# Kernel tuning notes

Hardware: AMD Instinct MI355X
Metric: run time of the kernel (lower is better)

Reference implementation:

```python
import jax, jax.numpy as jnp
import numpy as np

LATENT, HIDDEN, OUT, NBLOCKS, NITER, BATCH = 128, 256, 128, 4, 10, 65536

def setup_inputs() -> dict:
    key = jax.random.key(0)
    ks = jax.random.split(key, 7)
    s_in = 1.0 / np.sqrt(LATENT)
    s_h = 1.0 / np.sqrt(HIDDEN)
    return {
        "x": jax.random.normal(ks[0], (BATCH, LATENT), jnp.float32),
        "W_init": jax.random.uniform(ks[1], (LATENT, HIDDEN), jnp.float32, -s_in, s_in),
        "b_init": jnp.zeros((HIDDEN,), jnp.float32),
        "Wg1": jax.random.uniform(ks[2], (NBLOCKS, HIDDEN, HIDDEN), jnp.float32, -s_h, s_h),
        "bg1": jax.random.uniform(ks[3], (NBLOCKS, HIDDEN), jnp.float32, -s_h, s_h),
        "Wg2": jax.random.uniform(ks[4], (NBLOCKS, HIDDEN, HIDDEN), jnp.float32, -s_h, s_h),
        "bg2": jax.random.uniform(ks[5], (NBLOCKS, HIDDEN), jnp.float32, -s_h, s_h),
        "W_final": jax.random.uniform(ks[6], (HIDDEN, OUT), jnp.float32, -s_h, s_h),
        "b_final": jnp.zeros((OUT,), jnp.float32),
    }

def _block(y, W1, b1, W2, b2):
    # fixed-point iteration: x <- y - g(x), g = Linear-ReLU-Linear
    def step(x, _):
        g = jax.nn.relu(x @ W1 + b1) @ W2 + b2
        return y - g, None
    x, _ = jax.lax.scan(step, y, None, length=NITER)
    return x

def reference(x, W_init, b_init, Wg1, bg1, Wg2, bg2, W_final, b_final):
    h = x @ W_init + b_init  # [B, HIDDEN]
    def blk(h, params):
        W1, b1, W2, b2 = params
        return _block(h, W1, b1, W2, b2), None
    h, _ = jax.lax.scan(blk, h, (Wg1, bg1, Wg2, bg2))
    return h @ W_final + b_final
```

## Files before the change

### kernel.cpp

```cpp
#include <hip/hip_runtime.h>
#include <hip/hip_bf16.h>


#define B_TOTAL 65536
#define LATENT  128
#define HIDDEN  256
#define OUTD    128
#define NBLOCKS 4
#define NITER   10
#define MTILE   64
#define LDSP    264

typedef unsigned short u16;
typedef unsigned int   u32;
typedef u16    u16x4  __attribute__((ext_vector_type(4)));
typedef u16    u16x8  __attribute__((ext_vector_type(8)));
typedef __bf16 bf16x8 __attribute__((ext_vector_type(8)));
typedef float  f32x16 __attribute__((ext_vector_type(16)));

__device__ inline u16 f2b(float f){ __bf16 h=(__bf16)f; return __builtin_bit_cast(u16,h); }
__device__ inline float up_lo(u32 u){ return __builtin_bit_cast(float, u<<16); }
__device__ inline float up_hi(u32 u){ return __builtin_bit_cast(float, u & 0xffff0000u); }
__device__ inline u32 pk2(float lo, float hi){ return (u32)f2b(lo) | ((u32)f2b(hi)<<16); }

#define AGC \
 "a0","a1","a2","a3","a4","a5","a6","a7","a8","a9","a10","a11","a12","a13","a14","a15", \
 "a16","a17","a18","a19","a20","a21","a22","a23","a24","a25","a26","a27","a28","a29","a30","a31", \
 "a32","a33","a34","a35","a36","a37","a38","a39","a40","a41","a42","a43","a44","a45","a46","a47", \
 "a48","a49","a50","a51","a52","a53","a54","a55","a56","a57","a58","a59","a60","a61","a62","a63", \
 "a64","a65","a66","a67","a68","a69","a70","a71","a72","a73","a74","a75","a76","a77","a78","a79", \
 "a80","a81","a82","a83","a84","a85","a86","a87","a88","a89","a90","a91","a92","a93","a94","a95", \
 "a96","a97","a98","a99","a100","a101","a102","a103","a104","a105","a106","a107","a108","a109","a110","a111", \
 "a112","a113","a114","a115","a116","a117","a118","a119","a120","a121","a122","a123","a124","a125","a126","a127"

#define LOADW(P, KS, NEG, A0,A1,A2,A3) { \
  const float* _w = (P) + (size_t)((KS)*16 + hi*8)*HIDDEN + colw; \
  float _v0=_w[0], _v1=_w[HIDDEN], _v2=_w[2*HIDDEN], _v3=_w[3*HIDDEN]; \
  float _v4=_w[4*HIDDEN], _v5=_w[5*HIDDEN], _v6=_w[6*HIDDEN], _v7=_w[7*HIDDEN]; \
  if (NEG){_v0=-_v0;_v1=-_v1;_v2=-_v2;_v3=-_v3;_v4=-_v4;_v5=-_v5;_v6=-_v6;_v7=-_v7;} \
  u32 _d0=pk2(_v0,_v1), _d1=pk2(_v2,_v3), _d2=pk2(_v4,_v5), _d3=pk2(_v6,_v7); \
  asm volatile("v_accvgpr_write_b32 a" #A0 ", %0\n\t" \
               "v_accvgpr_write_b32 a" #A1 ", %1\n\t" \
               "v_accvgpr_write_b32 a" #A2 ", %2\n\t" \
               "v_accvgpr_write_b32 a" #A3 ", %3" \
               :: "v"(_d0),"v"(_d1),"v"(_d2),"v"(_d3) : AGC); }

#define STEP(SRC, KS, A0, A3) { \
  bf16x8 _b0 = *(const bf16x8*)((SRC) + rdA0 + (KS)*16); \
  bf16x8 _b1 = *(const bf16x8*)((SRC) + rdA1 + (KS)*16); \
  asm volatile("v_mfma_f32_32x32x16_bf16 %0, a[" #A0 ":" #A3 "], %1, %0" \
               : "+v"(acc0) : "v"(_b0) : AGC); \
  asm volatile("v_mfma_f32_32x32x16_bf16 %0, a[" #A0 ":" #A3 "], %1, %0" \
               : "+v"(acc1) : "v"(_b1) : AGC); }

#define ACCFENCE asm volatile("s_nop 7\n\ts_nop 7\n\ts_nop 7" : "+v"(acc0), "+v"(acc1))

#define MFMA_I(a,b,c) __builtin_amdgcn_mfma_f32_32x32x16_bf16(a,b,c,0,0,0)

__device__ inline bf16x8 load_wfrag_f(const float* __restrict__ W, int ldw, int krow0,
                                      int col){
  bf16x8 r;
#pragma unroll
  for (int j=0;j<8;j++) r[j] = (__bf16)W[(size_t)(krow0+j)*ldw + col];
  return r;
}

__device__ inline void store_tile(u16* __restrict__ dst, int row_elem, int nb, int hi,
                                  const f32x16 a, bool relu){
#pragma unroll
  for (int q=0;q<4;q++){
    u16x4 p;
#pragma unroll
    for (int i=0;i<4;i++){
      float v = a[4*q+i];
      if (relu) v = v > 0.f ? v : 0.f;
      p[i] = f2b(v);
    }
    *(u16x4*)(dst + row_elem + nb + 8*q + 4*hi) = p;
  }
}

__global__
__attribute__((amdgpu_flat_work_group_size(512,512)))
void irn_kernel(const float* __restrict__ x,
                const float* __restrict__ Winit, const float* __restrict__ binit,
                const float* __restrict__ Wg1,   const float* __restrict__ bg1,
                const float* __restrict__ Wg2,   const float* __restrict__ bg2,
                const float* __restrict__ Wfin,  const float* __restrict__ bfin,
                float* __restrict__ out)
{
  __shared__ u16 Xb[MTILE*LDSP];
  __shared__ u16 Hb[MTILE*LDSP];

  const int tid = threadIdx.x;
  const int wv  = tid >> 6;
  const int ln  = tid & 63;
  const int lo  = ln & 31;
  const int hi  = ln >> 5;
  const int row0 = blockIdx.x * MTILE;
  const int nb   = wv * 32;
  const int colw = nb + lo;

  {
    const int r  = tid >> 3;
    const int c0 = (tid & 7) * 16;
    const float4* src = (const float4*)(x + (size_t)(row0 + r)*LATENT + c0);
    u16x8 p0, p1;
#pragma unroll
    for (int i=0;i<2;i++){
      float4 a = src[i*2], b = src[i*2+1];
      u16x8& p = i ? p1 : p0;
      p[0]=f2b(a.x); p[1]=f2b(a.y); p[2]=f2b(a.z); p[3]=f2b(a.w);
      p[4]=f2b(b.x); p[5]=f2b(b.y); p[6]=f2b(b.z); p[7]=f2b(b.w);
    }
    u16* dst = Xb + r*LDSP + c0;
    *(u16x8*)(dst)   = p0;
    *(u16x8*)(dst+8) = p1;
  }

  const int rdA0 = lo*LDSP + hi*8;
  const int rdA1 = (32+lo)*LDSP + hi*8;

  u32 yp0[8], yp1[8];
  u32 b1p[8];

  __syncthreads();

  {
    bf16x8 wf[8];
#pragma unroll
    for (int ks=0; ks<8; ks++)
      wf[ks] = load_wfrag_f(Winit, HIDDEN, ks*16 + hi*8, colw);
    f32x16 acc0, acc1;
#pragma unroll
    for (int r=0;r<16;r++){
      float bv = binit[nb + (r&3) + 8*(r>>2) + 4*hi];
      acc0[r]=bv; acc1[r]=bv;
    }
#pragma unroll
    for (int ks=0; ks<8; ks++){
      bf16x8 b0 = *(const bf16x8*)(Xb + rdA0 + ks*16);
      bf16x8 b1 = *(const bf16x8*)(Xb + rdA1 + ks*16);
      acc0=MFMA_I(wf[ks], b0, acc0);
      acc1=MFMA_I(wf[ks], b1, acc1);
    }
    __syncthreads();
    store_tile(Xb, (0 +lo)*LDSP, nb, hi, acc0, false);
    store_tile(Xb, (32+lo)*LDSP, nb, hi, acc1, false);
#pragma unroll
    for (int i=0;i<8;i++){
      yp0[i] = pk2(acc0[2*i], acc0[2*i+1]);
      yp1[i] = pk2(acc1[2*i], acc1[2*i+1]);
    }
    __syncthreads();
  }

#pragma unroll 1
  for (int b=0; b<NBLOCKS; b++){
    const float* W1p = Wg1 + (size_t)b*HIDDEN*HIDDEN;
    const float* W2p = Wg2 + (size_t)b*HIDDEN*HIDDEN;

    LOADW(W1p, 0,0,  0,1,2,3)    LOADW(W1p, 1,0,  4,5,6,7)
    LOADW(W1p, 2,0,  8,9,10,11)  LOADW(W1p, 3,0,  12,13,14,15)
    LOADW(W1p, 4,0,  16,17,18,19) LOADW(W1p, 5,0,  20,21,22,23)
    LOADW(W1p, 6,0,  24,25,26,27) LOADW(W1p, 7,0,  28,29,30,31)
    LOADW(W1p, 8,0,  32,33,34,35) LOADW(W1p, 9,0,  36,37,38,39)
    LOADW(W1p,10,0,  40,41,42,43) LOADW(W1p,11,0,  44,45,46,47)
    LOADW(W1p,12,0,  48,49,50,51) LOADW(W1p,13,0,  52,53,54,55)
    LOADW(W1p,14,0,  56,57,58,59) LOADW(W1p,15,0,  60,61,62,63)
    LOADW(W2p, 0,1,  64,65,66,67)   LOADW(W2p, 1,1,  68,69,70,71)
    LOADW(W2p, 2,1,  72,73,74,75)   LOADW(W2p, 3,1,  76,77,78,79)
    LOADW(W2p, 4,1,  80,81,82,83)   LOADW(W2p, 5,1,  84,85,86,87)
    LOADW(W2p, 6,1,  88,89,90,91)   LOADW(W2p, 7,1,  92,93,94,95)
    LOADW(W2p, 8,1,  96,97,98,99)   LOADW(W2p, 9,1,  100,101,102,103)
    LOADW(W2p,10,1,  104,105,106,107) LOADW(W2p,11,1,  108,109,110,111)
    LOADW(W2p,12,1,  112,113,114,115) LOADW(W2p,13,1,  116,117,118,119)
    LOADW(W2p,14,1,  120,121,122,123) LOADW(W2p,15,1,  124,125,126,127)
    asm volatile("s_nop 3" :::);

    {
      const float* b1g = bg1 + b*HIDDEN;
      const float* b2g = bg2 + b*HIDDEN;
#pragma unroll
      for (int i=0;i<8;i++){
        const int c = nb + (2*i&3) + 8*(2*i>>2) + 4*hi;
        b1p[i] = pk2(b1g[c], b1g[c+1]);
        yp0[i] = pk2(up_lo(yp0[i]) - b2g[c], up_hi(yp0[i]) - b2g[c+1]);
        yp1[i] = pk2(up_lo(yp1[i]) - b2g[c], up_hi(yp1[i]) - b2g[c+1]);
      }
    }

#pragma unroll 1
    for (int it=0; it<NITER; it++){
      {
        f32x16 acc0, acc1;
#pragma unroll
        for (int i=0;i<8;i++){
          acc0[2*i]=up_lo(b1p[i]); acc0[2*i+1]=up_hi(b1p[i]);
          acc1[2*i]=acc0[2*i];     acc1[2*i+1]=acc0[2*i+1];
        }
        STEP(Xb, 0, 0,3)   STEP(Xb, 1, 4,7)   STEP(Xb, 2, 8,11)  STEP(Xb, 3, 12,15)
        STEP(Xb, 4, 16,19) STEP(Xb, 5, 20,23) STEP(Xb, 6, 24,27) STEP(Xb, 7, 28,31)
        STEP(Xb, 8, 32,35) STEP(Xb, 9, 36,39) STEP(Xb,10, 40,43) STEP(Xb,11, 44,47)
        STEP(Xb,12, 48,51) STEP(Xb,13, 52,55) STEP(Xb,14, 56,59) STEP(Xb,15, 60,63)
        ACCFENCE;
        store_tile(Hb, (0 +lo)*LDSP, nb, hi, acc0, true);
        store_tile(Hb, (32+lo)*LDSP, nb, hi, acc1, true);
      }
      __syncthreads();
      {
        f32x16 acc0, acc1;
#pragma unroll
        for (int i=0;i<8;i++){
          acc0[2*i]=up_lo(yp0[i]); acc0[2*i+1]=up_hi(yp0[i]);
          acc1[2*i]=up_lo(yp1[i]); acc1[2*i+1]=up_hi(yp1[i]);
        }
        STEP(Hb, 0, 64,67)   STEP(Hb, 1, 68,71)   STEP(Hb, 2, 72,75)   STEP(Hb, 3, 76,79)
        STEP(Hb, 4, 80,83)   STEP(Hb, 5, 84,87)   STEP(Hb, 6, 88,91)   STEP(Hb, 7, 92,95)
        STEP(Hb, 8, 96,99)   STEP(Hb, 9, 100,103) STEP(Hb,10, 104,107) STEP(Hb,11, 108,111)
        STEP(Hb,12, 112,115) STEP(Hb,13, 116,119) STEP(Hb,14, 120,123) STEP(Hb,15, 124,127)
        ACCFENCE;
        store_tile(Xb, (0 +lo)*LDSP, nb, hi, acc0, false);
        store_tile(Xb, (32+lo)*LDSP, nb, hi, acc1, false);
        if (it == NITER-1){
#pragma unroll
          for (int i=0;i<8;i++){
            yp0[i] = pk2(acc0[2*i], acc0[2*i+1]);
            yp1[i] = pk2(acc1[2*i], acc1[2*i+1]);
          }
        }
      }
      __syncthreads();
    }
  }

  {
    const int mf = (wv & 3) * 32;
    const int nf = (wv >> 2);
    const int rdF = (nf*32 + lo)*LDSP + hi*8;
    bf16x8 wf[16];
#pragma unroll
    for (int ks=0; ks<16; ks++)
      wf[ks] = load_wfrag_f(Wfin, OUTD, ks*16 + hi*8, mf + lo);
    f32x16 acc;
#pragma unroll
    for (int r=0;r<16;r++) acc[r] = bfin[mf + (r&3) + 8*(r>>2) + 4*hi];
#pragma unroll
    for (int ks=0; ks<16; ks++){
      bf16x8 bfr = *(const bf16x8*)(Xb + rdF + ks*16);
      acc = MFMA_I(wf[ks], bfr, acc);
    }
    float* orow = out + (size_t)(row0 + nf*32 + lo)*OUTD;
#pragma unroll
    for (int q=0;q<4;q++){
      float4 v = make_float4(acc[4*q], acc[4*q+1], acc[4*q+2], acc[4*q+3]);
      *(float4*)(orow + mf + 8*q + 4*hi) = v;
    }
  }
}

extern "C" void kernel_launch(void* const* d_in, const int* in_sizes, int n_in,
                              void* d_out, int out_size, void* d_ws, size_t ws_size,
                              hipStream_t stream) {
  (void)in_sizes; (void)n_in; (void)d_ws; (void)ws_size; (void)out_size;
  const float* x     = (const float*)d_in[0];
  const float* Winit = (const float*)d_in[1];
  const float* binit = (const float*)d_in[2];
  const float* Wg1   = (const float*)d_in[3];
  const float* bg1   = (const float*)d_in[4];
  const float* Wg2   = (const float*)d_in[5];
  const float* bg2   = (const float*)d_in[6];
  const float* Wfin  = (const float*)d_in[7];
  const float* bfin  = (const float*)d_in[8];
  float* out = (float*)d_out;
  irn_kernel<<<dim3(B_TOTAL/MTILE), dim3(512), 0, stream>>>(
      x, Winit, binit, Wg1, bg1, Wg2, bg2, Wfin, bfin, out);
}
```

Measured before the change: 768.4 us.

## Halve workgroup to 4 waves, each computing a 64x64 output tile

The workgroup shrinks from 8 waves to 4, and each wave now handles 64 output columns (two 32-column weight fragments) instead of 32. This doubles MFMA work per wave for every LDS B-fragment read, cutting LDS read traffic per FLOP. The hand-written AGPR inline-asm weight pinning is replaced with compiler-managed register arrays: 64 bf16x8 weight fragments per wave, plus waves_per_eu(1,1) so the compiler can use the full register file. The risks are register spills, lower occupancy, and the loss of explicit AGPR placement.

```diff
diff --git a/kernel.cpp b/kernel.cpp
--- a/kernel.cpp
+++ b/kernel.cpp
@@ -23,39 +23,17 @@
 __device__ inline float up_hi(u32 u){ return __builtin_bit_cast(float, u & 0xffff0000u); }
 __device__ inline u32 pk2(float lo, float hi){ return (u32)f2b(lo) | ((u32)f2b(hi)<<16); }
 
-#define AGC \
- "a0","a1","a2","a3","a4","a5","a6","a7","a8","a9","a10","a11","a12","a13","a14","a15", \
- "a16","a17","a18","a19","a20","a21","a22","a23","a24","a25","a26","a27","a28","a29","a30","a31", \
- "a32","a33","a34","a35","a36","a37","a38","a39","a40","a41","a42","a43","a44","a45","a46","a47", \
- "a48","a49","a50","a51","a52","a53","a54","a55","a56","a57","a58","a59","a60","a61","a62","a63", \
- "a64","a65","a66","a67","a68","a69","a70","a71","a72","a73","a74","a75","a76","a77","a78","a79", \
- "a80","a81","a82","a83","a84","a85","a86","a87","a88","a89","a90","a91","a92","a93","a94","a95", \
- "a96","a97","a98","a99","a100","a101","a102","a103","a104","a105","a106","a107","a108","a109","a110","a111", \
- "a112","a113","a114","a115","a116","a117","a118","a119","a120","a121","a122","a123","a124","a125","a126","a127"
-
-#define LOADW(P, KS, NEG, A0,A1,A2,A3) { \
-  const float* _w = (P) + (size_t)((KS)*16 + hi*8)*HIDDEN + colw; \
-  float _v0=_w[0], _v1=_w[HIDDEN], _v2=_w[2*HIDDEN], _v3=_w[3*HIDDEN]; \
-  float _v4=_w[4*HIDDEN], _v5=_w[5*HIDDEN], _v6=_w[6*HIDDEN], _v7=_w[7*HIDDEN]; \
-  if (NEG){_v0=-_v0;_v1=-_v1;_v2=-_v2;_v3=-_v3;_v4=-_v4;_v5=-_v5;_v6=-_v6;_v7=-_v7;} \
-  u32 _d0=pk2(_v0,_v1), _d1=pk2(_v2,_v3), _d2=pk2(_v4,_v5), _d3=pk2(_v6,_v7); \
-  asm volatile("v_accvgpr_write_b32 a" #A0 ", %0\n\t" \
-               "v_accvgpr_write_b32 a" #A1 ", %1\n\t" \
-               "v_accvgpr_write_b32 a" #A2 ", %2\n\t" \
-               "v_accvgpr_write_b32 a" #A3 ", %3" \
-               :: "v"(_d0),"v"(_d1),"v"(_d2),"v"(_d3) : AGC); }
-
-#define STEP(SRC, KS, A0, A3) { \
-  bf16x8 _b0 = *(const bf16x8*)((SRC) + rdA0 + (KS)*16); \
-  bf16x8 _b1 = *(const bf16x8*)((SRC) + rdA1 + (KS)*16); \
-  asm volatile("v_mfma_f32_32x32x16_bf16 %0, a[" #A0 ":" #A3 "], %1, %0" \
-               : "+v"(acc0) : "v"(_b0) : AGC); \
-  asm volatile("v_mfma_f32_32x32x16_bf16 %0, a[" #A0 ":" #A3 "], %1, %0" \
-               : "+v"(acc1) : "v"(_b1) : AGC); }
-
-#define ACCFENCE asm volatile("s_nop 7\n\ts_nop 7\n\ts_nop 7" : "+v"(acc0), "+v"(acc1))
-
 #define MFMA_I(a,b,c) __builtin_amdgcn_mfma_f32_32x32x16_bf16(a,b,c,0,0,0)
+
+__device__ inline bf16x8 wfrag(const float* __restrict__ W, int krow0, int col, bool neg){
+  bf16x8 r;
+#pragma unroll
+  for (int j=0;j<8;j++){
+    float v = W[(size_t)(krow0+j)*HIDDEN + col];
+    r[j] = (__bf16)(neg ? -v : v);
+  }
+  return r;
+}
 
 __device__ inline bf16x8 load_wfrag_f(const float* __restrict__ W, int ldw, int krow0,
                                       int col){
@@ -65,7 +43,7 @@
   return r;
 }
 
-__device__ inline void store_tile(u16* __restrict__ dst, int row_elem, int nb, int hi,
+__device__ inline void store_tile(u16* __restrict__ dst, int row_elem, int colbase, int hi,
                                   const f32x16 a, bool relu){
 #pragma unroll
   for (int q=0;q<4;q++){
@@ -76,12 +54,12 @@
       if (relu) v = v > 0.f ? v : 0.f;
       p[i] = f2b(v);
     }
-    *(u16x4*)(dst + row_elem + nb + 8*q + 4*hi) = p;
+    *(u16x4*)(dst + row_elem + colbase + 8*q + 4*hi) = p;
   }
 }
 
 __global__
-__attribute__((amdgpu_flat_work_group_size(512,512)))
+__attribute__((amdgpu_flat_work_group_size(256,256), amdgpu_waves_per_eu(1,1)))
 void irn_kernel(const float* __restrict__ x,
                 const float* __restrict__ Winit, const float* __restrict__ binit,
                 const float* __restrict__ Wg1,   const float* __restrict__ bg1,
@@ -98,59 +76,69 @@
   const int lo  = ln & 31;
   const int hi  = ln >> 5;
   const int row0 = blockIdx.x * MTILE;
-  const int nb   = wv * 32;
-  const int colw = nb + lo;
+  const int nb   = wv * 64;
+  const int colw0 = nb + lo;
+  const int colw1 = nb + 32 + lo;
 
   {
-    const int r  = tid >> 3;
-    const int c0 = (tid & 7) * 16;
+    const int r  = tid >> 2;
+    const int c0 = (tid & 3) * 32;
     const float4* src = (const float4*)(x + (size_t)(row0 + r)*LATENT + c0);
-    u16x8 p0, p1;
-#pragma unroll
-    for (int i=0;i<2;i++){
+    u16* dst = Xb + r*LDSP + c0;
+#pragma unroll
+    for (int i=0;i<4;i++){
       float4 a = src[i*2], b = src[i*2+1];
-      u16x8& p = i ? p1 : p0;
+      u16x8 p;
       p[0]=f2b(a.x); p[1]=f2b(a.y); p[2]=f2b(a.z); p[3]=f2b(a.w);
       p[4]=f2b(b.x); p[5]=f2b(b.y); p[6]=f2b(b.z); p[7]=f2b(b.w);
-    }
-    u16* dst = Xb + r*LDSP + c0;
-    *(u16x8*)(dst)   = p0;
-    *(u16x8*)(dst+8) = p1;
+      *(u16x8*)(dst + i*8) = p;
+    }
   }
 
   const int rdA0 = lo*LDSP + hi*8;
   const int rdA1 = (32+lo)*LDSP + hi*8;
 
-  u32 yp0[8], yp1[8];
-  u32 b1p[8];
+  u32 yp00[8], yp10[8], yp01[8], yp11[8];
+  u32 b1p0[8], b1p1[8];
 
   __syncthreads();
 
   {
-    bf16x8 wf[8];
-#pragma unroll
-    for (int ks=0; ks<8; ks++)
-      wf[ks] = load_wfrag_f(Winit, HIDDEN, ks*16 + hi*8, colw);
-    f32x16 acc0, acc1;
+    bf16x8 wf0[8], wf1[8];
+#pragma unroll
+    for (int ks=0; ks<8; ks++){
+      wf0[ks] = load_wfrag_f(Winit, HIDDEN, ks*16 + hi*8, colw0);
+      wf1[ks] = load_wfrag_f(Winit, HIDDEN, ks*16 + hi*8, colw1);
+    }
+    f32x16 acc00, acc10, acc01, acc11;
 #pragma unroll
     for (int r=0;r<16;r++){
-      float bv = binit[nb + (r&3) + 8*(r>>2) + 4*hi];
-      acc0[r]=bv; acc1[r]=bv;
+      const int cm = (r&3) + 8*(r>>2) + 4*hi;
+      float bv0 = binit[nb + cm];
+      float bv1 = binit[nb + 32 + cm];
+      acc00[r]=bv0; acc10[r]=bv0;
+      acc01[r]=bv1; acc11[r]=bv1;
     }
 #pragma unroll
     for (int ks=0; ks<8; ks++){
       bf16x8 b0 = *(const bf16x8*)(Xb + rdA0 + ks*16);
       bf16x8 b1 = *(const bf16x8*)(Xb + rdA1 + ks*16);
-      acc0=MFMA_I(wf[ks], b0, acc0);
-      acc1=MFMA_I(wf[ks], b1, acc1);
+      acc00=MFMA_I(wf0[ks], b0, acc00);
+      acc10=MFMA_I(wf0[ks], b1, acc10);
+      acc01=MFMA_I(wf1[ks], b0, acc01);
+      acc11=MFMA_I(wf1[ks], b1, acc11);
     }
     __syncthreads();
-    store_tile(Xb, (0 +lo)*LDSP, nb, hi, acc0, false);
-    store_tile(Xb, (32+lo)*LDSP, nb, hi, acc1, false);
+    store_tile(Xb, (0 +lo)*LDSP, nb,    hi, acc00, false);
+    store_tile(Xb, (32+lo)*LDSP, nb,    hi, acc10, false);
+    store_tile(Xb, (0 +lo)*LDSP, nb+32, hi, acc01, false);
+    store_tile(Xb, (32+lo)*LDSP, nb+32, hi, acc11, false);
 #pragma unroll
     for (int i=0;i<8;i++){
-      yp0[i] = pk2(acc0[2*i], acc0[2*i+1]);
-      yp1[i] = pk2(acc1[2*i], acc1[2*i+1]);
+      yp00[i] = pk2(acc00[2*i], acc00[2*i+1]);
+      yp10[i] = pk2(acc10[2*i], acc10[2*i+1]);
+      yp01[i] = pk2(acc01[2*i], acc01[2*i+1]);
+      yp11[i] = pk2(acc11[2*i], acc11[2*i+1]);
     }
     __syncthreads();
   }
@@ -160,73 +148,87 @@
     const float* W1p = Wg1 + (size_t)b*HIDDEN*HIDDEN;
     const float* W2p = Wg2 + (size_t)b*HIDDEN*HIDDEN;
 
-    LOADW(W1p, 0,0,  0,1,2,3)    LOADW(W1p, 1,0,  4,5,6,7)
-    LOADW(W1p, 2,0,  8,9,10,11)  LOADW(W1p, 3,0,  12,13,14,15)
-    LOADW(W1p, 4,0,  16,17,18,19) LOADW(W1p, 5,0,  20,21,22,23)
-    LOADW(W1p, 6,0,  24,25,26,27) LOADW(W1p, 7,0,  28,29,30,31)
-    LOADW(W1p, 8,0,  32,33,34,35) LOADW(W1p, 9,0,  36,37,38,39)
-    LOADW(W1p,10,0,  40,41,42,43) LOADW(W1p,11,0,  44,45,46,47)
-    LOADW(W1p,12,0,  48,49,50,51) LOADW(W1p,13,0,  52,53,54,55)
-    LOADW(W1p,14,0,  56,57,58,59) LOADW(W1p,15,0,  60,61,62,63)
-    LOADW(W2p, 0,1,  64,65,66,67)   LOADW(W2p, 1,1,  68,69,70,71)
-    LOADW(W2p, 2,1,  72,73,74,75)   LOADW(W2p, 3,1,  76,77,78,79)
-    LOADW(W2p, 4,1,  80,81,82,83)   LOADW(W2p, 5,1,  84,85,86,87)
-    LOADW(W2p, 6,1,  88,89,90,91)   LOADW(W2p, 7,1,  92,93,94,95)
-    LOADW(W2p, 8,1,  96,97,98,99)   LOADW(W2p, 9,1,  100,101,102,103)
-    LOADW(W2p,10,1,  104,105,106,107) LOADW(W2p,11,1,  108,109,110,111)
-    LOADW(W2p,12,1,  112,113,114,115) LOADW(W2p,13,1,  116,117,118,119)
-    LOADW(W2p,14,1,  120,121,122,123) LOADW(W2p,15,1,  124,125,126,127)
-    asm volatile("s_nop 3" :::);
+    bf16x8 wA[16], wB[16], wC[16], wD[16];
+#pragma unroll
+    for (int ks=0; ks<16; ks++){
+      const int kr = ks*16 + hi*8;
+      wA[ks] = wfrag(W1p, kr, colw0, false);
+      wB[ks] = wfrag(W1p, kr, colw1, false);
+      wC[ks] = wfrag(W2p, kr, colw0, true);
+      wD[ks] = wfrag(W2p, kr, colw1, true);
+    }
 
     {
       const float* b1g = bg1 + b*HIDDEN;
       const float* b2g = bg2 + b*HIDDEN;
 #pragma unroll
       for (int i=0;i<8;i++){
-        const int c = nb + (2*i&3) + 8*(2*i>>2) + 4*hi;
-        b1p[i] = pk2(b1g[c], b1g[c+1]);
-        yp0[i] = pk2(up_lo(yp0[i]) - b2g[c], up_hi(yp0[i]) - b2g[c+1]);
-        yp1[i] = pk2(up_lo(yp1[i]) - b2g[c], up_hi(yp1[i]) - b2g[c+1]);
+        const int cm = (2*i&3) + 8*(2*i>>2) + 4*hi;
+        const int c0 = nb + cm, c1 = nb + 32 + cm;
+        b1p0[i] = pk2(b1g[c0], b1g[c0+1]);
+        b1p1[i] = pk2(b1g[c1], b1g[c1+1]);
+        yp00[i] = pk2(up_lo(yp00[i]) - b2g[c0], up_hi(yp00[i]) - b2g[c0+1]);
+        yp10[i] = pk2(up_lo(yp10[i]) - b2g[c0], up_hi(yp10[i]) - b2g[c0+1]);
+        yp01[i] = pk2(up_lo(yp01[i]) - b2g[c1], up_hi(yp01[i]) - b2g[c1+1]);
+        yp11[i] = pk2(up_lo(yp11[i]) - b2g[c1], up_hi(yp11[i]) - b2g[c1+1]);
       }
     }
 
 #pragma unroll 1
     for (int it=0; it<NITER; it++){
       {
-        f32x16 acc0, acc1;
+        f32x16 acc00, acc10, acc01, acc11;
 #pragma unroll
         for (int i=0;i<8;i++){
-          acc0[2*i]=up_lo(b1p[i]); acc0[2*i+1]=up_hi(b1p[i]);
-          acc1[2*i]=acc0[2*i];     acc1[2*i+1]=acc0[2*i+1];
-        }
-        STEP(Xb, 0, 0,3)   STEP(Xb, 1, 4,7)   STEP(Xb, 2, 8,11)  STEP(Xb, 3, 12,15)
-        STEP(Xb, 4, 16,19) STEP(Xb, 5, 20,23) STEP(Xb, 6, 24,27) STEP(Xb, 7, 28,31)
-        STEP(Xb, 8, 32,35) STEP(Xb, 9, 36,39) STEP(Xb,10, 40,43) STEP(Xb,11, 44,47)
-        STEP(Xb,12, 48,51) STEP(Xb,13, 52,55) STEP(Xb,14, 56,59) STEP(Xb,15, 60,63)
-        ACCFENCE;
-        store_tile(Hb, (0 +lo)*LDSP, nb, hi, acc0, true);
-        store_tile(Hb, (32+lo)*LDSP, nb, hi, acc1, true);
+          acc00[2*i]=up_lo(b1p0[i]); acc00[2*i+1]=up_hi(b1p0[i]);
+          acc10[2*i]=acc00[2*i];     acc10[2*i+1]=acc00[2*i+1];
+          acc01[2*i]=up_lo(b1p1[i]); acc01[2*i+1]=up_hi(b1p1[i]);
+          acc11[2*i]=acc01[2*i];     acc11[2*i+1]=acc01[2*i+1];
+        }
+#pragma unroll
+        for (int ks=0; ks<16; ks++){
+          bf16x8 b0 = *(const bf16x8*)(Xb + rdA0 + ks*16);
+          bf16x8 b1 = *(const bf16x8*)(Xb + rdA1 + ks*16);
+          acc00 = MFMA_I(wA[ks], b0, acc00);
+          acc10 = MFMA_I(wA[ks], b1, acc10);
+          acc01 = MFMA_I(wB[ks], b0, acc01);
+          acc11 = MFMA_I(wB[ks], b1, acc11);
+        }
+        store_tile(Hb, (0 +lo)*LDSP, nb,    hi, acc00, true);
+        store_tile(Hb, (32+lo)*LDSP, nb,    hi, acc10, true);
+        store_tile(Hb, (0 +lo)*LDSP, nb+32, hi, acc01, true);
+        store_tile(Hb, (32+lo)*LDSP, nb+32, hi, acc11, true);
       }
       __syncthreads();
       {
-        f32x16 acc0, acc1;
+        f32x16 acc00, acc10, acc01, acc11;
 #pragma unroll
         for (int i=0;i<8;i++){
-          acc0[2*i]=up_lo(yp0[i]); acc0[2*i+1]=up_hi(yp0[i]);
-          acc1[2*i]=up_lo(yp1[i]); acc1[2*i+1]=up_hi(yp1[i]);
-        }
-        STEP(Hb, 0, 64,67)   STEP(Hb, 1, 68,71)   STEP(Hb, 2, 72,75)   STEP(Hb, 3, 76,79)
-        STEP(Hb, 4, 80,83)   STEP(Hb, 5, 84,87)   STEP(Hb, 6, 88,91)   STEP(Hb, 7, 92,95)
-        STEP(Hb, 8, 96,99)   STEP(Hb, 9, 100,103) STEP(Hb,10, 104,107) STEP(Hb,11, 108,111)
-        STEP(Hb,12, 112,115) STEP(Hb,13, 116,119) STEP(Hb,14, 120,123) STEP(Hb,15, 124,127)
-        ACCFENCE;
-        store_tile(Xb, (0 +lo)*LDSP, nb, hi, acc0, false);
-        store_tile(Xb, (32+lo)*LDSP, nb, hi, acc1, false);
+          acc00[2*i]=up_lo(yp00[i]); acc00[2*i+1]=up_hi(yp00[i]);
+          acc10[2*i]=up_lo(yp10[i]); acc10[2*i+1]=up_hi(yp10[i]);
+          acc01[2*i]=up_lo(yp01[i]); acc01[2*i+1]=up_hi(yp01[i]);
+          acc11[2*i]=up_lo(yp11[i]); acc11[2*i+1]=up_hi(yp11[i]);
+        }
+#pragma unroll
+        for (int ks=0; ks<16; ks++){
+          bf16x8 b0 = *(const bf16x8*)(Hb + rdA0 + ks*16);
+          bf16x8 b1 = *(const bf16x8*)(Hb + rdA1 + ks*16);
+          acc00 = MFMA_I(wC[ks], b0, acc00);
+          acc10 = MFMA_I(wC[ks], b1, acc10);
+          acc01 = MFMA_I(wD[ks], b0, acc01);
+          acc11 = MFMA_I(wD[ks], b1, acc11);
+        }
+        store_tile(Xb, (0 +lo)*LDSP, nb,    hi, acc00, false);
+        store_tile(Xb, (32+lo)*LDSP, nb,    hi, acc10, false);
+        store_tile(Xb, (0 +lo)*LDSP, nb+32, hi, acc01, false);
+        store_tile(Xb, (32+lo)*LDSP, nb+32, hi, acc11, false);
         if (it == NITER-1){
 #pragma unroll
           for (int i=0;i<8;i++){
-            yp0[i] = pk2(acc0[2*i], acc0[2*i+1]);
-            yp1[i] = pk2(acc1[2*i], acc1[2*i+1]);
+            yp00[i] = pk2(acc00[2*i], acc00[2*i+1]);
+            yp10[i] = pk2(acc10[2*i], acc10[2*i+1]);
+            yp01[i] = pk2(acc01[2*i], acc01[2*i+1]);
+            yp11[i] = pk2(acc11[2*i], acc11[2*i+1]);
           }
         }
       }
@@ -235,26 +237,32 @@
   }
 
   {
-    const int mf = (wv & 3) * 32;
-    const int nf = (wv >> 2);
-    const int rdF = (nf*32 + lo)*LDSP + hi*8;
+    const int mf = wv * 32;
     bf16x8 wf[16];
 #pragma unroll
     for (int ks=0; ks<16; ks++)
       wf[ks] = load_wfrag_f(Wfin, OUTD, ks*16 + hi*8, mf + lo);
-    f32x16 acc;
-#pragma unroll
-    for (int r=0;r<16;r++) acc[r] = bfin[mf + (r&3) + 8*(r>>2) + 4*hi];
+    f32x16 acc0, acc1;
+#pragma unroll
+    for (int r=0;r<16;r++){
+      float bv = bfin[mf + (r&3) + 8*(r>>2) + 4*hi];
+      acc0[r] = bv; acc1[r] = bv;
+    }
 #pragma unroll
     for (int ks=0; ks<16; ks++){
-      bf16x8 bfr = *(const bf16x8*)(Xb + rdF + ks*16);
-      acc = MFMA_I(wf[ks], bfr, acc);
-    }
-    float* orow = out + (size_t)(row0 + nf*32 + lo)*OUTD;
+      bf16x8 b0 = *(const bf16x8*)(Xb + rdA0 + ks*16);
+      bf16x8 b1 = *(const bf16x8*)(Xb + rdA1 + ks*16);
+      acc0 = MFMA_I(wf[ks], b0, acc0);
+      acc1 = MFMA_I(wf[ks], b1, acc1);
+    }
+    float* orow0 = out + (size_t)(row0 +      lo)*OUTD;
+    float* orow1 = out + (size_t)(row0 + 32 + lo)*OUTD;
 #pragma unroll
     for (int q=0;q<4;q++){
-      float4 v = make_float4(acc[4*q], acc[4*q+1], acc[4*q+2], acc[4*q+3]);
-      *(float4*)(orow + mf + 8*q + 4*hi) = v;
+      float4 v0 = make_float4(acc0[4*q], acc0[4*q+1], acc0[4*q+2], acc0[4*q+3]);
+      float4 v1 = make_float4(acc1[4*q], acc1[4*q+1], acc1[4*q+2], acc1[4*q+3]);
+      *(float4*)(orow0 + mf + 8*q + 4*hi) = v0;
+      *(float4*)(orow1 + mf + 8*q + 4*hi) = v1;
     }
   }
 }
@@ -273,6 +281,6 @@
   const float* Wfin  = (const float*)d_in[7];
   const float* bfin  = (const float*)d_in[8];
   float* out = (float*)d_out;
-  irn_kernel<<<dim3(B_TOTAL/MTILE), dim3(512), 0, stream>>>(
+  irn_kernel<<<dim3(B_TOTAL/MTILE), dim3(256), 0, stream>>>(
       x, Winit, binit, Wg1, bg1, Wg2, bg2, Wfin, bfin, out);
 }
```

New measurement: 1.240 ms. +61.4%, slower.
